# Kernel optimization log

Measured on AMD Instinct MI355X. Metric: run time of the kernel, lower is better.

The kernel has to match this reference:

```python
import jax, jax.numpy as jnp
import numpy as np

N = 4096  # query nodes
L = 4096  # source nodes
C = 512   # in_channels == out_channels (required by the original code path)
H = 8     # num_heads
DK = C // H  # 64


def setup_inputs() -> dict:
    key = jax.random.key(0)
    ks = jax.random.split(key, 12)
    s = 1.0 / np.sqrt(C)
    return {
        "query_input": jax.random.normal(ks[0], (N, C), jnp.float32),
        "source_input": jax.random.normal(ks[1], (L, C), jnp.float32),
        # outer value projection (TransConvLayerGAT.Wv): C -> C
        "Wv_out_w": jax.random.uniform(ks[2], (C, C), jnp.float32, -s, s),
        "Wv_out_b": jax.random.uniform(ks[3], (C,), jnp.float32, -s, s),
        # attention projections
        "Wq_w": jax.random.uniform(ks[4], (C, H * DK), jnp.float32, -s, s),
        "Wq_b": jax.random.uniform(ks[5], (H * DK,), jnp.float32, -s, s),
        "Wk_w": jax.random.uniform(ks[6], (C, H * DK), jnp.float32, -s, s),
        "Wk_b": jax.random.uniform(ks[7], (H * DK,), jnp.float32, -s, s),
        # attention value projection: C -> H * out_channels
        "Wv_attn_w": jax.random.uniform(ks[8], (C, H * C), jnp.float32, -s, s),
        "Wv_attn_b": jax.random.uniform(ks[9], (H * C,), jnp.float32, -s, s),
    }


def reference(query_input, source_input, Wv_out_w, Wv_out_b,
              Wq_w, Wq_b, Wk_w, Wk_b, Wv_attn_w, Wv_attn_b):
    # outer value projection (use_weight=True)
    value = source_input @ Wv_out_w + Wv_out_b            # [L, C]
    # attention projections
    q = (query_input @ Wq_w + Wq_b).reshape(N, H, DK)     # [N, H, DK]
    k = (source_input @ Wk_w + Wk_b).reshape(L, H, DK)    # [L, H, DK]
    v = (value @ Wv_attn_w + Wv_attn_b).reshape(L, H, C)  # [L, H, C]
    scale = 1.0 / jnp.sqrt(jnp.float32(DK))
    scores = jnp.einsum('nhm,lhm->nlh', q, k) * scale     # [N, L, H]
    # NOTE: faithful to original — softmax over the HEADS axis (dim=-1)
    w = jax.nn.softmax(scores, axis=-1)                   # [N, L, H]
    out = jnp.einsum('nlh,lhd->nhd', w, v)                # [N, H, C]
    return out
```

## Files before the change

kernel.cpp:

```cpp
#include <hip/hip_runtime.h>
#include <cstddef>
#include <cstdint>

#define NQ 4096
#define NS 4096
#define CH 512
#define NH 8
#define HC 4096

typedef unsigned short u16;
typedef __attribute__((ext_vector_type(8))) short short8;
typedef __attribute__((ext_vector_type(4))) float f32x4;

__device__ __forceinline__ u16 f2b(float f) {
  unsigned u = __float_as_uint(f);
  return (u16)((u + 0x7fffu + ((u >> 16) & 1u)) >> 16);
}
__device__ __forceinline__ float b2f(u16 h) {
  return __uint_as_float(((unsigned)h) << 16);
}
__device__ __forceinline__ f32x4 mfma16(short8 a, short8 b, f32x4 c) {
  return __builtin_amdgcn_mfma_f32_16x16x32_bf16(a, b, c, 0, 0, 0);
}
__device__ __forceinline__ void gload_lds16(const void* g, void* l) {
  __builtin_amdgcn_global_load_lds(
      (const __attribute__((address_space(1))) void*)g,
      (__attribute__((address_space(3))) void*)l, 16, 0, 0);
}

__global__ __launch_bounds__(256) void convert_flat(
    const float* __restrict__ in, u16* __restrict__ out, int n4)
{
  int idx = blockIdx.x * 256 + threadIdx.x;
  int stride = gridDim.x * 256;
  for (int i = idx; i < n4; i += stride) {
    float4 v = ((const float4*)in)[i];
    ushort4 o;
    o.x = f2b(v.x); o.y = f2b(v.y); o.z = f2b(v.z); o.w = f2b(v.w);
    ((ushort4*)out)[i] = o;
  }
}

__global__ __launch_bounds__(256) void transpose_convert(
    const float* __restrict__ in, u16* __restrict__ out, int R, int C)
{
  __shared__ u16 tile[32][33];
  int tid = threadIdx.x;
  int tx = tid & 31, ty = tid >> 5;
#pragma unroll
  for (int i = 0; i < 4; ++i) {
    int r = blockIdx.y * 32 + ty + i * 8;
    int c = blockIdx.x * 32 + tx;
    tile[ty + i * 8][tx] = f2b(in[(size_t)r * C + c]);
  }
  __syncthreads();
#pragma unroll
  for (int i = 0; i < 4; ++i) {
    int co = blockIdx.x * 32 + ty + i * 8;
    int ro = blockIdx.y * 32 + tx;
    out[(size_t)co * R + ro] = tile[tx][ty + i * 8];
  }
}

template <int MODE>
__global__ __launch_bounds__(256) void gemm_core(
    const u16* __restrict__ A, int lda,
    const u16* __restrict__ Bt, int ldb,
    u16* __restrict__ Cb, float* __restrict__ Cf, int ldc,
    const float* __restrict__ bias, float* __restrict__ sl,
    int K, size_t aPlane)
{
  constexpr int BM = (MODE == 2) ? 32 : 128;
  constexpr int BN = (MODE == 2) ? 256 : 128;
  constexpr int WC = (MODE == 2) ? 4 : 2;
  constexpr int FM = (MODE == 2) ? 2 : 4;
  constexpr int FN = (MODE == 2) ? 4 : 4;
  constexpr int ABYTES = BM * 64;
  constexpr int NCH = (BM + BN) * 64 / 1024;

  __shared__ u16 smem[(BM + BN) * 32];
  u16* As = smem;
  u16* Bs = smem + BM * 32;

  const int tid = threadIdx.x;
  const int wid = tid >> 6, lane = tid & 63;
  const int wr = wid / WC, wc = wid % WC;
  const int fr = wr * FM * 16, fc = wc * FN * 16;
  const int m0 = blockIdx.y * BM, n0 = blockIdx.x * BN;
  const int bz = blockIdx.z;

  if constexpr (MODE == 2) { A += (size_t)bz * aPlane; Cb += (size_t)bz * 512; }
  if constexpr (MODE == 3) {
    A += (size_t)bz * 512; Bt += (size_t)bz * 512 * 512;
    bias += (size_t)bz * 512; Cf += (size_t)bz * 512;
  }

  f32x4 acc[FM][FN];
#pragma unroll
  for (int m = 0; m < FM; ++m)
#pragma unroll
    for (int n = 0; n < FN; ++n)
#pragma unroll
      for (int i = 0; i < 4; ++i) acc[m][n][i] = 0.f;

  float rowsum = 0.f;
  const int lcol = (lane & 3) << 3;
  const int lrow4 = lane >> 2;

  for (int k0 = 0; k0 < K; k0 += 32) {
    for (int c = wid; c < NCH; c += 4) {
      int boff = c << 10;
      const u16* g;
      if (boff < ABYTES) {
        int r = (boff >> 6) + lrow4;
        g = A + (size_t)(m0 + r) * lda + (k0 + lcol);
      } else {
        int r = ((boff - ABYTES) >> 6) + lrow4;
        g = Bt + (size_t)(n0 + r) * ldb + (k0 + lcol);
      }
      gload_lds16(g, (char*)smem + boff);
    }
    __syncthreads();

    if constexpr (MODE == 2) {
      if (blockIdx.x == 0 && tid < BM) {
        float r = 0.f;
#pragma unroll
        for (int j = 0; j < 32; ++j) r += b2f(As[tid * 32 + j]);
        rowsum += r;
      }
    }

    short8 af[FM], bq[FN];
    const int kg = (lane >> 4) << 3;
#pragma unroll
    for (int m = 0; m < FM; ++m)
      af[m] = *(const short8*)(As + (size_t)(fr + m * 16 + (lane & 15)) * 32 + kg);
#pragma unroll
    for (int n = 0; n < FN; ++n)
      bq[n] = *(const short8*)(Bs + (size_t)(fc + n * 16 + (lane & 15)) * 32 + kg);
#pragma unroll
    for (int m = 0; m < FM; ++m)
#pragma unroll
      for (int n = 0; n < FN; ++n)
        acc[m][n] = mfma16(af[m], bq[n], acc[m][n]);
    __syncthreads();
  }

  const int crow = (lane >> 4) << 2;
  const int ccol = lane & 15;

  if constexpr (MODE == 0) {
#pragma unroll
    for (int n = 0; n < FN; ++n) {
      int gn = n0 + fc + n * 16 + ccol;
      float bv = bias[gn];
#pragma unroll
      for (int m = 0; m < FM; ++m)
#pragma unroll
        for (int i = 0; i < 4; ++i) {
          int gm = m0 + fr + m * 16 + crow + i;
          Cb[(size_t)gm * ldc + gn] = f2b(acc[m][n][i] + bv);
        }
    }
  } else if constexpr (MODE == 1) {
#pragma unroll
    for (int n = 0; n < FN; ++n) {
      int gn = n0 + fc + n * 16 + ccol;
      float bv = bias[gn];
#pragma unroll
      for (int m = 0; m < FM; ++m) {
        int mb = m0 + fr + m * 16 + crow;
        ushort4 o;
        o.x = f2b(acc[m][n][0] + bv); o.y = f2b(acc[m][n][1] + bv);
        o.z = f2b(acc[m][n][2] + bv); o.w = f2b(acc[m][n][3] + bv);
        *(ushort4*)(Cb + (size_t)gn * ldc + mb) = o;
      }
    }
  } else if constexpr (MODE == 2) {
#pragma unroll
    for (int m = 0; m < FM; ++m)
#pragma unroll
      for (int i = 0; i < 4; ++i) {
        int gm = m0 + fr + m * 16 + crow + i;
#pragma unroll
        for (int n = 0; n < FN; ++n) {
          int gn = n0 + fc + n * 16 + ccol;
          Cb[(size_t)gm * ldc + gn] = f2b(acc[m][n][i]);
        }
      }
    if (blockIdx.x == 0 && tid < BM) sl[(size_t)(m0 + tid) * 8 + bz] = rowsum;
  } else {
#pragma unroll
    for (int m = 0; m < FM; ++m)
#pragma unroll
      for (int i = 0; i < 4; ++i) {
        int gm = m0 + fr + m * 16 + crow + i;
        float slv = sl[(size_t)gm * 8 + bz];
#pragma unroll
        for (int n = 0; n < FN; ++n) {
          int gn = n0 + fc + n * 16 + ccol;
          Cf[(size_t)gm * ldc + gn] = acc[m][n][i] + slv * bias[gn];
        }
      }
  }
}

__global__ __launch_bounds__(256) void attn_pass1(
    const u16* __restrict__ q, const u16* __restrict__ kmat,
    u16* __restrict__ W, int nbase, size_t plane)
{
  const int tid = threadIdx.x, wid = tid >> 6, lane = tid & 63;
  const int n0 = nbase + blockIdx.y * 16;
  const int l0 = blockIdx.x * 128 + wid * 32;
  const int r16 = lane & 15, kg = (lane >> 4) << 3;

  f32x4 acc[8][2];
#pragma unroll
  for (int h = 0; h < 8; ++h)
#pragma unroll
    for (int f = 0; f < 2; ++f)
#pragma unroll
      for (int i = 0; i < 4; ++i) acc[h][f][i] = 0.f;

  const u16* qrow = q + (size_t)(n0 + r16) * CH + kg;
  const u16* k0p = kmat + (size_t)(l0 + r16) * CH + kg;
  const u16* k1p = k0p + (size_t)16 * CH;

#pragma unroll
  for (int h = 0; h < 8; ++h) {
#pragma unroll
    for (int kk = 0; kk < 2; ++kk) {
      int off = h * 64 + kk * 32;
      short8 a  = *(const short8*)(qrow + off);
      short8 b0 = *(const short8*)(k0p + off);
      short8 b1 = *(const short8*)(k1p + off);
      acc[h][0] = mfma16(a, b0, acc[h][0]);
      acc[h][1] = mfma16(a, b1, acc[h][1]);
    }
  }

  const int rowl = blockIdx.y * 16 + ((lane >> 4) << 2);
#pragma unroll
  for (int f = 0; f < 2; ++f) {
#pragma unroll
    for (int i = 0; i < 4; ++i) {
      float s[8], mx = -3e38f;
#pragma unroll
      for (int h = 0; h < 8; ++h) { s[h] = acc[h][f][i] * 0.125f; mx = fmaxf(mx, s[h]); }
      float sum = 0.f;
#pragma unroll
      for (int h = 0; h < 8; ++h) { s[h] = __expf(s[h] - mx); sum += s[h]; }
      float inv = 1.0f / sum;
      size_t base = (size_t)(rowl + i) * NS + l0 + f * 16 + (lane & 15);
#pragma unroll
      for (int h = 0; h < 8; ++h) W[(size_t)h * plane + base] = f2b(s[h] * inv);
    }
  }
}

extern "C" void kernel_launch(void* const* d_in, const int* in_sizes, int n_in,
                              void* d_out, int out_size, void* d_ws, size_t ws_size,
                              hipStream_t stream)
{
  const float* query   = (const float*)d_in[0];
  const float* source  = (const float*)d_in[1];
  const float* Wvo_w   = (const float*)d_in[2];
  const float* Wvo_b   = (const float*)d_in[3];
  const float* Wq_w    = (const float*)d_in[4];
  const float* Wq_b    = (const float*)d_in[5];
  const float* Wk_w    = (const float*)d_in[6];
  const float* Wk_b    = (const float*)d_in[7];
  const float* Wva_w   = (const float*)d_in[8];
  const float* Wva_b   = (const float*)d_in[9];
  float* out = (float*)d_out;

  char* base = (char*)d_ws;
  size_t o = 0;
  auto alloc = [&](size_t b) -> char* {
    char* p = base + o;
    o += (b + 255) & ~(size_t)255;
    return p;
  };
  u16* query_bf  = (u16*)alloc((size_t)NQ * CH * 2);
  u16* source_bf = (u16*)alloc((size_t)NS * CH * 2);
  u16* WqT  = (u16*)alloc((size_t)CH * CH * 2);
  u16* WkT  = (u16*)alloc((size_t)CH * CH * 2);
  u16* WvoT = (u16*)alloc((size_t)CH * CH * 2);
  u16* WvaT = (u16*)alloc((size_t)CH * HC * 2);
  u16* qb   = (u16*)alloc((size_t)NQ * CH * 2);
  u16* kb   = (u16*)alloc((size_t)NS * CH * 2);
  u16* valT = (u16*)alloc((size_t)CH * NS * 2);
  u16* Tb   = (u16*)alloc((size_t)NQ * HC * 2);
  float* slb = (float*)alloc((size_t)NQ * NH * 4);
  size_t fixed = o;

  int c = 16;
  for (int cand = 1; cand <= 16; cand <<= 1) {
    if (fixed + (size_t)8 * (NQ / cand) * NS * 2 <= ws_size) { c = cand; break; }
  }
  const int rows = NQ / c;
  u16* Wb = (u16*)alloc((size_t)8 * rows * NS * 2);
  const size_t plane = (size_t)rows * NS;

  convert_flat<<<1024, 256, 0, stream>>>(query, query_bf, NQ * CH / 4);
  convert_flat<<<1024, 256, 0, stream>>>(source, source_bf, NS * CH / 4);
  transpose_convert<<<dim3(16, 16), 256, 0, stream>>>(Wq_w, WqT, CH, CH);
  transpose_convert<<<dim3(16, 16), 256, 0, stream>>>(Wk_w, WkT, CH, CH);
  transpose_convert<<<dim3(16, 16), 256, 0, stream>>>(Wvo_w, WvoT, CH, CH);
  transpose_convert<<<dim3(128, 16), 256, 0, stream>>>(Wva_w, WvaT, CH, HC);

  gemm_core<0><<<dim3(4, 32), 256, 0, stream>>>(query_bf, CH, WqT, CH, qb, nullptr, CH,
                                                Wq_b, nullptr, CH, 0);
  gemm_core<0><<<dim3(4, 32), 256, 0, stream>>>(source_bf, CH, WkT, CH, kb, nullptr, CH,
                                                Wk_b, nullptr, CH, 0);
  gemm_core<1><<<dim3(4, 32), 256, 0, stream>>>(source_bf, CH, WvoT, CH, valT, nullptr, NS,
                                                Wvo_b, nullptr, CH, 0);

  for (int ci = 0; ci < c; ++ci) {
    int nb = ci * rows;
    attn_pass1<<<dim3(32, rows / 16), 256, 0, stream>>>(qb, kb, Wb, nb, plane);
    gemm_core<2><<<dim3(2, rows / 32, 8), 256, 0, stream>>>(
        Wb, NS, valT, NS, Tb + (size_t)nb * HC, nullptr, HC,
        nullptr, slb + (size_t)nb * NH, NS, plane);
  }

  gemm_core<3><<<dim3(4, 32, 8), 256, 0, stream>>>(
      Tb, HC, WvaT, CH, nullptr, out, HC, Wva_b, slb, CH, 0);
}
```

Measured before the change: 716.1 us.

## Fold attention value projection ahead of attention GEMM and stage softmax writes through LDS

The attention value projection (value @ Wv_attn + bias) is now computed once into a transposed per-head V2 matrix, so the attention GEMM writes the final output directly. This removes the separate intermediate T buffer, the row-sum bookkeeping used for the bias, and the final per-head projection GEMM. The attention GEMM now uses the square 128x128 tile instead of the narrow 32x256 one. attn_pass1 keeps Q fragments in registers and stages the softmax weights in swizzled shared memory so the global stores are coalesced 16-byte writes. Total FLOPs stay about the same, but an extra 4096x4096 bf16 intermediate is materialized.

```diff
diff --git a/kernel.cpp b/kernel.cpp
--- a/kernel.cpp
+++ b/kernel.cpp
@@ -15,9 +15,6 @@
 __device__ __forceinline__ u16 f2b(float f) {
   unsigned u = __float_as_uint(f);
   return (u16)((u + 0x7fffu + ((u >> 16) & 1u)) >> 16);
-}
-__device__ __forceinline__ float b2f(u16 h) {
-  return __uint_as_float(((unsigned)h) << 16);
 }
 __device__ __forceinline__ f32x4 mfma16(short8 a, short8 b, f32x4 c) {
   return __builtin_amdgcn_mfma_f32_16x16x32_bf16(a, b, c, 0, 0, 0);
@@ -67,14 +64,11 @@
     const u16* __restrict__ A, int lda,
     const u16* __restrict__ Bt, int ldb,
     u16* __restrict__ Cb, float* __restrict__ Cf, int ldc,
-    const float* __restrict__ bias, float* __restrict__ sl,
+    const float* __restrict__ bias,
     int K, size_t aPlane)
 {
-  constexpr int BM = (MODE == 2) ? 32 : 128;
-  constexpr int BN = (MODE == 2) ? 256 : 128;
-  constexpr int WC = (MODE == 2) ? 4 : 2;
-  constexpr int FM = (MODE == 2) ? 2 : 4;
-  constexpr int FN = (MODE == 2) ? 4 : 4;
+  constexpr int BM = 128, BN = 128;
+  constexpr int FM = 4, FN = 4;
   constexpr int ABYTES = BM * 64;
   constexpr int NCH = (BM + BN) * 64 / 1024;
 
@@ -84,15 +78,15 @@
 
   const int tid = threadIdx.x;
   const int wid = tid >> 6, lane = tid & 63;
-  const int wr = wid / WC, wc = wid % WC;
+  const int wr = wid >> 1, wc = wid & 1;
   const int fr = wr * FM * 16, fc = wc * FN * 16;
   const int m0 = blockIdx.y * BM, n0 = blockIdx.x * BN;
-  const int bz = blockIdx.z;
-
-  if constexpr (MODE == 2) { A += (size_t)bz * aPlane; Cb += (size_t)bz * 512; }
+
   if constexpr (MODE == 3) {
-    A += (size_t)bz * 512; Bt += (size_t)bz * 512 * 512;
-    bias += (size_t)bz * 512; Cf += (size_t)bz * 512;
+    const int bz = blockIdx.z;
+    A += (size_t)bz * aPlane;
+    Bt += (size_t)bz * 512 * ldb;
+    Cf += (size_t)bz * 512;
   }
 
   f32x4 acc[FM][FN];
@@ -103,7 +97,6 @@
 #pragma unroll
       for (int i = 0; i < 4; ++i) acc[m][n][i] = 0.f;
 
-  float rowsum = 0.f;
   const int lcol = (lane & 3) << 3;
   const int lrow4 = lane >> 2;
 
@@ -122,15 +115,6 @@
     }
     __syncthreads();
 
-    if constexpr (MODE == 2) {
-      if (blockIdx.x == 0 && tid < BM) {
-        float r = 0.f;
-#pragma unroll
-        for (int j = 0; j < 32; ++j) r += b2f(As[tid * 32 + j]);
-        rowsum += r;
-      }
-    }
-
     short8 af[FM], bq[FN];
     const int kg = (lane >> 4) << 3;
 #pragma unroll
@@ -177,7 +161,7 @@
         *(ushort4*)(Cb + (size_t)gn * ldc + mb) = o;
       }
     }
-  } else if constexpr (MODE == 2) {
+  } else {
 #pragma unroll
     for (int m = 0; m < FM; ++m)
 #pragma unroll
@@ -186,21 +170,7 @@
 #pragma unroll
         for (int n = 0; n < FN; ++n) {
           int gn = n0 + fc + n * 16 + ccol;
-          Cb[(size_t)gm * ldc + gn] = f2b(acc[m][n][i]);
-        }
-      }
-    if (blockIdx.x == 0 && tid < BM) sl[(size_t)(m0 + tid) * 8 + bz] = rowsum;
-  } else {
-#pragma unroll
-    for (int m = 0; m < FM; ++m)
-#pragma unroll
-      for (int i = 0; i < 4; ++i) {
-        int gm = m0 + fr + m * 16 + crow + i;
-        float slv = sl[(size_t)gm * 8 + bz];
-#pragma unroll
-        for (int n = 0; n < FN; ++n) {
-          int gn = n0 + fc + n * 16 + ccol;
-          Cf[(size_t)gm * ldc + gn] = acc[m][n][i] + slv * bias[gn];
+          Cf[(size_t)gm * ldc + gn] = acc[m][n][i];
         }
       }
   }
@@ -210,10 +180,23 @@
     const u16* __restrict__ q, const u16* __restrict__ kmat,
     u16* __restrict__ W, int nbase, size_t plane)
 {
+  __shared__ u16 lbuf[16384];
+  char* lb = (char*)lbuf;
+
   const int tid = threadIdx.x, wid = tid >> 6, lane = tid & 63;
-  const int n0 = nbase + blockIdx.y * 16;
-  const int l0 = blockIdx.x * 128 + wid * 32;
-  const int r16 = lane & 15, kg = (lane >> 4) << 3;
+  const int nloc0 = blockIdx.y * 16;
+  const int l0 = blockIdx.x * 128;
+  const int lw = l0 + wid * 32;
+  const int r16 = lane & 15, g = lane >> 4;
+  const int kg = g << 3;
+
+  short8 qf[16];
+  const u16* qrow = q + (size_t)(nbase + nloc0 + r16) * CH + kg;
+#pragma unroll
+  for (int h = 0; h < 8; ++h)
+#pragma unroll
+    for (int kk = 0; kk < 2; ++kk)
+      qf[h * 2 + kk] = *(const short8*)(qrow + h * 64 + kk * 32);
 
   f32x4 acc[8][2];
 #pragma unroll
@@ -223,26 +206,22 @@
 #pragma unroll
       for (int i = 0; i < 4; ++i) acc[h][f][i] = 0.f;
 
-  const u16* qrow = q + (size_t)(n0 + r16) * CH + kg;
-  const u16* k0p = kmat + (size_t)(l0 + r16) * CH + kg;
-  const u16* k1p = k0p + (size_t)16 * CH;
-
-#pragma unroll
-  for (int h = 0; h < 8; ++h) {
-#pragma unroll
-    for (int kk = 0; kk < 2; ++kk) {
-      int off = h * 64 + kk * 32;
-      short8 a  = *(const short8*)(qrow + off);
-      short8 b0 = *(const short8*)(k0p + off);
-      short8 b1 = *(const short8*)(k1p + off);
-      acc[h][0] = mfma16(a, b0, acc[h][0]);
-      acc[h][1] = mfma16(a, b1, acc[h][1]);
-    }
-  }
-
-  const int rowl = blockIdx.y * 16 + ((lane >> 4) << 2);
 #pragma unroll
   for (int f = 0; f < 2; ++f) {
+    const u16* krow = kmat + (size_t)(lw + f * 16 + r16) * CH + kg;
+#pragma unroll
+    for (int h = 0; h < 8; ++h)
+#pragma unroll
+      for (int kk = 0; kk < 2; ++kk) {
+        short8 kf = *(const short8*)(krow + h * 64 + kk * 32);
+        acc[h][f] = mfma16(kf, qf[h * 2 + kk], acc[h][f]);
+      }
+  }
+
+  const int nn = r16;
+#pragma unroll
+  for (int f = 0; f < 2; ++f) {
+    u16 wb[4][8];
 #pragma unroll
     for (int i = 0; i < 4; ++i) {
       float s[8], mx = -3e38f;
@@ -252,10 +231,28 @@
 #pragma unroll
       for (int h = 0; h < 8; ++h) { s[h] = __expf(s[h] - mx); sum += s[h]; }
       float inv = 1.0f / sum;
-      size_t base = (size_t)(rowl + i) * NS + l0 + f * 16 + (lane & 15);
-#pragma unroll
-      for (int h = 0; h < 8; ++h) W[(size_t)h * plane + base] = f2b(s[h] * inv);
-    }
+#pragma unroll
+      for (int h = 0; h < 8; ++h) wb[i][h] = f2b(s[h] * inv);
+    }
+    const int lloc = wid * 32 + f * 16 + g * 4;
+#pragma unroll
+    for (int h = 0; h < 8; ++h) {
+      unsigned p0 = (unsigned)wb[0][h] | ((unsigned)wb[1][h] << 16);
+      unsigned p1 = (unsigned)wb[2][h] | ((unsigned)wb[3][h] << 16);
+      int wa = (h << 12) + (nn << 8) + (lloc << 1);
+      wa ^= (nn & 7) << 4;
+      *(uint2*)(lb + wa) = make_uint2(p0, p1);
+    }
+  }
+  __syncthreads();
+
+  const int rn = tid >> 4, rl = (tid & 15) << 3;
+#pragma unroll
+  for (int h = 0; h < 8; ++h) {
+    int ra = (h << 12) + (rn << 8) + (rl << 1);
+    ra ^= (rn & 7) << 4;
+    uint4 v = *(const uint4*)(lb + ra);
+    *(uint4*)(W + (size_t)h * plane + (size_t)(nloc0 + rn) * NS + l0 + rl) = v;
   }
 }
 
@@ -290,17 +287,16 @@
   u16* WvaT = (u16*)alloc((size_t)CH * HC * 2);
   u16* qb   = (u16*)alloc((size_t)NQ * CH * 2);
   u16* kb   = (u16*)alloc((size_t)NS * CH * 2);
-  u16* valT = (u16*)alloc((size_t)CH * NS * 2);
-  u16* Tb   = (u16*)alloc((size_t)NQ * HC * 2);
-  float* slb = (float*)alloc((size_t)NQ * NH * 4);
+  u16* valr = (u16*)alloc((size_t)NS * CH * 2);
+  u16* V2T  = (u16*)alloc((size_t)HC * NS * 2);
   size_t fixed = o;
 
-  int c = 16;
-  for (int cand = 1; cand <= 16; cand <<= 1) {
-    if (fixed + (size_t)8 * (NQ / cand) * NS * 2 <= ws_size) { c = cand; break; }
+  int c = 32;
+  for (int cand = 1; cand <= 32; cand <<= 1) {
+    if (fixed + (size_t)NH * (NQ / cand) * NS * 2 <= ws_size) { c = cand; break; }
   }
   const int rows = NQ / c;
-  u16* Wb = (u16*)alloc((size_t)8 * rows * NS * 2);
+  u16* Wb = (u16*)alloc((size_t)NH * rows * NS * 2);
   const size_t plane = (size_t)rows * NS;
 
   convert_flat<<<1024, 256, 0, stream>>>(query, query_bf, NQ * CH / 4);
@@ -311,20 +307,19 @@
   transpose_convert<<<dim3(128, 16), 256, 0, stream>>>(Wva_w, WvaT, CH, HC);
 
   gemm_core<0><<<dim3(4, 32), 256, 0, stream>>>(query_bf, CH, WqT, CH, qb, nullptr, CH,
-                                                Wq_b, nullptr, CH, 0);
+                                                Wq_b, CH, 0);
   gemm_core<0><<<dim3(4, 32), 256, 0, stream>>>(source_bf, CH, WkT, CH, kb, nullptr, CH,
-                                                Wk_b, nullptr, CH, 0);
-  gemm_core<1><<<dim3(4, 32), 256, 0, stream>>>(source_bf, CH, WvoT, CH, valT, nullptr, NS,
-                                                Wvo_b, nullptr, CH, 0);
+                                                Wk_b, CH, 0);
+  gemm_core<0><<<dim3(4, 32), 256, 0, stream>>>(source_bf, CH, WvoT, CH, valr, nullptr, CH,
+                                                Wvo_b, CH, 0);
+
+  gemm_core<1><<<dim3(32, 32), 256, 0, stream>>>(valr, CH, WvaT, CH, V2T, nullptr, NS,
+                                                 Wva_b, CH, 0);
 
   for (int ci = 0; ci < c; ++ci) {
-    int nb = ci * rows;
+    const int nb = ci * rows;
     attn_pass1<<<dim3(32, rows / 16), 256, 0, stream>>>(qb, kb, Wb, nb, plane);
-    gemm_core<2><<<dim3(2, rows / 32, 8), 256, 0, stream>>>(
-        Wb, NS, valT, NS, Tb + (size_t)nb * HC, nullptr, HC,
-        nullptr, slb + (size_t)nb * NH, NS, plane);
-  }
-
-  gemm_core<3><<<dim3(4, 32, 8), 256, 0, stream>>>(
-      Tb, HC, WvaT, CH, nullptr, out, HC, Wva_b, slb, CH, 0);
-}
+    gemm_core<3><<<dim3(4, rows / 128, 8), 256, 0, stream>>>(
+        Wb, NS, V2T, NS, nullptr, out + (size_t)nb * HC, HC, nullptr, NS, plane);
+  }
+}
```

Result: faster. 677.3 us (-5.4%).
